# Kernel optimization log

Measured on AMD Instinct MI355X. Metric: run time of the kernel, lower is better.

## Reference

```python
import jax, jax.numpy as jnp
import numpy as np

D_MODEL = 1024
N_HEADS = 16
HEAD_DIM = D_MODEL // N_HEADS  # 64


def _rotate_half(x):
    x1, x2 = jnp.split(x, 2, axis=-1)
    return jnp.concatenate((-x2, x1), axis=-1)


def setup_inputs() -> dict:
    key = jax.random.key(0)
    ks = jax.random.split(key, 9)
    B, S = 2, 2048
    sc = 1.0 / np.sqrt(D_MODEL)
    return {
        "x": jax.random.normal(ks[0], (B, S, D_MODEL), dtype=jnp.float32),
        "Wq": jax.random.normal(ks[1], (D_MODEL, D_MODEL), dtype=jnp.float32) * sc,
        "bq": jax.random.normal(ks[2], (D_MODEL,), dtype=jnp.float32) * 0.02,
        "Wk": jax.random.normal(ks[3], (D_MODEL, D_MODEL), dtype=jnp.float32) * sc,
        "bk": jax.random.normal(ks[4], (D_MODEL,), dtype=jnp.float32) * 0.02,
        "Wv": jax.random.normal(ks[5], (D_MODEL, D_MODEL), dtype=jnp.float32) * sc,
        "bv": jax.random.normal(ks[6], (D_MODEL,), dtype=jnp.float32) * 0.02,
        "Wo": jax.random.normal(ks[7], (D_MODEL, D_MODEL), dtype=jnp.float32) * sc,
        "bo": jax.random.normal(ks[8], (D_MODEL,), dtype=jnp.float32) * 0.02,
    }


def reference(x, Wq, bq, Wk, bk, Wv, bv, Wo, bo):
    B, S, _ = x.shape
    H, D = N_HEADS, HEAD_DIM
    # QKV projections -> [B, H, S, D]
    q = (x @ Wq + bq).reshape(B, S, H, D).transpose(0, 2, 1, 3)
    k = (x @ Wk + bk).reshape(B, S, H, D).transpose(0, 2, 1, 3)
    v = (x @ Wv + bv).reshape(B, S, H, D).transpose(0, 2, 1, 3)
    # Rotary embedding on head_dim
    inv_freq = 1.0 / (10000.0 ** (jnp.arange(0, D, 2, dtype=jnp.float32) / D))
    t = jnp.arange(S, dtype=jnp.float32)
    freqs = jnp.outer(t, inv_freq)                      # [S, D/2]
    emb = jnp.concatenate((freqs, freqs), axis=-1)      # [S, D]
    # Faithful to torch: cos/sin end up rank-5 [1,1,1,S,D], promoting q/k to [1,B,H,S,D]
    cos = jnp.cos(emb)[None, None, None]
    sin = jnp.sin(emb)[None, None, None]
    qe = q * cos + _rotate_half(q) * sin                # [1,B,H,S,D]
    ke = k * cos + _rotate_half(k) * sin                # [1,B,H,S,D]
    scores = jnp.matmul(qe, jnp.swapaxes(ke, -1, -2)) / np.sqrt(D).astype(np.float32)  # [1,B,H,S,S]
    attn = jax.nn.softmax(scores, axis=-1)
    out = jnp.matmul(attn, v)                           # [1,B,H,S,D] (v broadcast)
    # Faithful replication of torch transpose(1,2).contiguous().view(B,S,d_model)
    out = out.transpose(0, 2, 1, 3, 4).reshape(B, S, H * D)
    return out @ Wo + bo
```

## Files before the change

kernel.cpp:

```cpp
#include <hip/hip_runtime.h>
#include <hip/hip_bf16.h>
#include <stdint.h>

typedef __bf16 bf16;
typedef __bf16 bf16x8 __attribute__((ext_vector_type(8)));
typedef __bf16 bf16x4 __attribute__((ext_vector_type(4)));
typedef float  f32x4  __attribute__((ext_vector_type(4)));
typedef int    i32x4  __attribute__((ext_vector_type(4)));

#define MFMA16(a, b, c) __builtin_amdgcn_mfma_f32_16x16x32_bf16((a), (b), (c), 0, 0, 0)

#define GLOAD16(gp, lp) __builtin_amdgcn_global_load_lds(                     \
    (__attribute__((address_space(1))) void*)(gp),                            \
    (__attribute__((address_space(3))) void*)(lp), 16, 0, 0)


__global__ __launch_bounds__(256) void k_prep(
    const float* __restrict__ x,
    const float* __restrict__ Wq, const float* __restrict__ Wk,
    const float* __restrict__ Wv, const float* __restrict__ Wo,
    bf16* __restrict__ xb, bf16* __restrict__ wqkvt, bf16* __restrict__ wot,
    float* __restrict__ ct, float* __restrict__ st) {
    __shared__ float t[32][33];
    const int bid = blockIdx.x, tid = threadIdx.x;
    if (bid < 4096) {
        const int i = bid * 256 + tid;
        float4 v = ((const float4*)x)[i];
        bf16x4 o;
        o[0] = (bf16)v.x; o[1] = (bf16)v.y; o[2] = (bf16)v.z; o[3] = (bf16)v.w;
        ((bf16x4*)xb)[i] = o;
    } else if (bid < 4352) {
        const int i = (bid - 4096) * 256 + tid;
        const int s = i >> 5, j = i & 31;
        const float inv = expf(-(float)j * (9.210340371976184f / 32.0f));
        const float a = (float)s * inv;
        ct[i] = cosf(a);
        st[i] = sinf(a);
    } else {
        const int wb = bid - 4352;
        const int z = wb >> 10, tb = wb & 1023;
        const float* src = (z == 0) ? Wq : (z == 1) ? Wk : (z == 2) ? Wv : Wo;
        bf16* dst = (z < 3) ? wqkvt + (size_t)z * 1024 * 1024 : wot;
        const int bx = (tb & 31) * 32, by = (tb >> 5) * 32;
        const int tx = tid & 31, ty = tid >> 5;
#pragma unroll
        for (int i = 0; i < 32; i += 8)
            t[ty + i][tx] = src[(size_t)(by + ty + i) * 1024 + bx + tx];
        __syncthreads();
#pragma unroll
        for (int i = 0; i < 32; i += 8)
            dst[(size_t)(bx + ty + i) * 1024 + by + tx] = (bf16)t[tx][ty + i];
    }
}

__global__ __launch_bounds__(512) void k_gemm_qkv(
    const bf16* __restrict__ X, const bf16* __restrict__ Wt,
    const float* __restrict__ bq, const float* __restrict__ bk,
    const float* __restrict__ bv,
    const float* __restrict__ ct, const float* __restrict__ st,
    bf16* __restrict__ qbuf, bf16* __restrict__ kbuf, bf16* __restrict__ vtb) {
    __shared__ __align__(16) bf16 As[2 * 16384];
    __shared__ __align__(16) bf16 Bs[2 * 16384];
    f32x4 acc[8][4] = {};

    const int wg = blockIdx.x;
    const int sw = (wg & 7) * 24 + (wg >> 3);
    const int m0 = (sw / 12) * 256, n0 = (sw % 12) * 256;

    const int tid = threadIdx.x;
    const int w = tid >> 6, lane = tid & 63;
    const int wm = w >> 2, wn = w & 3;
    const int l15 = lane & 15, l4 = lane >> 4;
    const int skol = 8 * ((lane & 7) ^ (lane >> 3));
    const int c0   = (8 * l4) ^ (8 * (l15 & 7));

    const bf16* Ap = X  + (size_t)(m0 + (tid >> 3)) * 1024 + skol;
    const bf16* Bp = Wt + (size_t)(n0 + (tid >> 3)) * 1024 + skol;
    bf16* Ad = As + tid * 8;
    bf16* Bd = Bs + tid * 8;
    const bf16* pA0 = As + (wm * 128 + l15) * 64 + c0;
    const bf16* pA1 = As + (wm * 128 + l15) * 64 + (c0 ^ 32);
    const bf16* pB0 = Bs + (wn * 64 + l15) * 64 + c0;
    const bf16* pB1 = Bs + (wn * 64 + l15) * 64 + (c0 ^ 32);

#define ASTG(B, kt) do {                                                     \
        GLOAD16(Ap + (kt),          Ad + (B) * 16384);                       \
        GLOAD16(Ap + 65536 + (kt),  Ad + (B) * 16384 + 4096);                \
        GLOAD16(Ap + 131072 + (kt), Ad + (B) * 16384 + 8192);                \
        GLOAD16(Ap + 196608 + (kt), Ad + (B) * 16384 + 12288);               \
    } while (0)
#define BSTG(B, kt) do {                                                     \
        GLOAD16(Bp + (kt),          Bd + (B) * 16384);                       \
        GLOAD16(Bp + 65536 + (kt),  Bd + (B) * 16384 + 4096);                \
        GLOAD16(Bp + 131072 + (kt), Bd + (B) * 16384 + 8192);                \
        GLOAD16(Bp + 196608 + (kt), Bd + (B) * 16384 + 12288);               \
    } while (0)

#define QTILE(t, B) do {                                                      \
        asm volatile("s_waitcnt vmcnt(0)" ::: "memory");                      \
        __builtin_amdgcn_s_barrier();                                         \
        bf16x8 af[8][2], bfv[4][2];                                           \
             \
        _Pragma("unroll")                                                     \
        for (int m = 0; m < 4; ++m) {                                         \
            af[m][0] = *(const bf16x8*)(pA0 + (B) * 16384 + m * 1024);        \
            af[m][1] = *(const bf16x8*)(pA1 + (B) * 16384 + m * 1024);        \
        }                                                                     \
        _Pragma("unroll")                                                     \
        for (int n = 0; n < 2; ++n) {                                         \
            bfv[n][0] = *(const bf16x8*)(pB0 + (B) * 16384 + n * 1024);       \
            bfv[n][1] = *(const bf16x8*)(pB1 + (B) * 16384 + n * 1024);       \
        }                                                                     \
        if ((t) < 15) ASTG((B) ^ 1, ((t) + 1) * 64);                          \
        __builtin_amdgcn_s_setprio(1);                                        \
        _Pragma("unroll")                                                     \
        for (int m = 0; m < 4; ++m)                                           \
            _Pragma("unroll")                                                 \
            for (int n = 0; n < 2; ++n) {                                     \
                acc[m][n] = MFMA16(af[m][0], bfv[n][0], acc[m][n]);           \
                acc[m][n] = MFMA16(af[m][1], bfv[n][1], acc[m][n]);           \
            }                                                                 \
        __builtin_amdgcn_s_setprio(0);                                        \
        __builtin_amdgcn_s_barrier();                                         \
                       \
        _Pragma("unroll")                                                     \
        for (int n = 2; n < 4; ++n) {                                         \
            bfv[n][0] = *(const bf16x8*)(pB0 + (B) * 16384 + n * 1024);       \
            bfv[n][1] = *(const bf16x8*)(pB1 + (B) * 16384 + n * 1024);       \
        }                                                                     \
        if ((t) < 15) BSTG((B) ^ 1, ((t) + 1) * 64);                          \
        __builtin_amdgcn_s_setprio(1);                                        \
        _Pragma("unroll")                                                     \
        for (int m = 0; m < 4; ++m)                                           \
            _Pragma("unroll")                                                 \
            for (int n = 2; n < 4; ++n) {                                     \
                acc[m][n] = MFMA16(af[m][0], bfv[n][0], acc[m][n]);           \
                acc[m][n] = MFMA16(af[m][1], bfv[n][1], acc[m][n]);           \
            }                                                                 \
        __builtin_amdgcn_s_setprio(0);                                        \
        __builtin_amdgcn_s_barrier();                                         \
                                      \
        _Pragma("unroll")                                                     \
        for (int m = 4; m < 8; ++m) {                                         \
            af[m][0] = *(const bf16x8*)(pA0 + (B) * 16384 + m * 1024);        \
            af[m][1] = *(const bf16x8*)(pA1 + (B) * 16384 + m * 1024);        \
        }                                                                     \
        __builtin_amdgcn_s_setprio(1);                                        \
        _Pragma("unroll")                                                     \
        for (int m = 4; m < 8; ++m)                                           \
            _Pragma("unroll")                                                 \
            for (int n = 2; n < 4; ++n) {                                     \
                acc[m][n] = MFMA16(af[m][0], bfv[n][0], acc[m][n]);           \
                acc[m][n] = MFMA16(af[m][1], bfv[n][1], acc[m][n]);           \
            }                                                                 \
        __builtin_amdgcn_s_setprio(0);                                        \
        __builtin_amdgcn_s_barrier();                                         \
                     \
        __builtin_amdgcn_s_setprio(1);                                        \
        _Pragma("unroll")                                                     \
        for (int m = 4; m < 8; ++m)                                           \
            _Pragma("unroll")                                                 \
            for (int n = 0; n < 2; ++n) {                                     \
                acc[m][n] = MFMA16(af[m][0], bfv[n][0], acc[m][n]);           \
                acc[m][n] = MFMA16(af[m][1], bfv[n][1], acc[m][n]);           \
            }                                                                 \
        __builtin_amdgcn_s_setprio(0);                                        \
    } while (0)

    ASTG(0, 0);
    BSTG(0, 0);
    for (int t = 0; t < 16; t += 2) {
        QTILE(t, 0);
        QTILE(t + 1, 1);
    }
#undef QTILE
#undef BSTG
#undef ASTG

    const int featbase = n0 + wn * 64;
    const int kind = featbase >> 10;
    const int col0 = featbase & 1023;
    const int h = col0 >> 6;
    const float* bias = (kind == 0) ? bq : (kind == 1) ? bk : bv;
    const float oscale = (kind == 0) ? 0.18033688011112042f : 1.0f;

#pragma unroll
    for (int m = 0; m < 8; ++m) {
#pragma unroll
        for (int j = 0; j < 4; ++j) {
            const int tok = m0 + wm * 128 + 16 * m + 4 * l4 + j;
            const int b = tok >> 11, s = tok & 2047;
            float vals[4];
#pragma unroll
            for (int n = 0; n < 4; ++n)
                vals[n] = acc[m][n][j] + bias[col0 + 16 * n + l15];
            if (kind < 2) {
                bf16* dst = (kind == 0) ? qbuf : kbuf;
                const size_t base = ((size_t)((b * 16 + h) * 2048 + s)) * 64;
#pragma unroll
                for (int n = 0; n < 4; ++n) {
                    const int dd = 16 * n + l15;
                    const int jr = dd & 31;
                    const float c = ct[s * 32 + jr], sn = st[s * 32 + jr];
                    const float other = vals[n ^ 2];
                    const float rot = (dd < 32) ? -other : other;
                    dst[base + dd] = (bf16)((vals[n] * c + rot * sn) * oscale);
                }
            } else {
                const int sp = (s & ~63) | ((s & 0x1C) << 1) | ((s & 0x20) >> 3) | (s & 3);
#pragma unroll
                for (int n = 0; n < 4; ++n) {
                    const int dd = 16 * n + l15;
                    vtb[((size_t)((b * 16 + h) * 64 + dd)) * 2048 + sp] = (bf16)vals[n];
                }
            }
        }
    }
}

__global__ __launch_bounds__(512) void k_attn(const bf16* __restrict__ qbuf,
                                              const bf16* __restrict__ kbuf,
                                              const bf16* __restrict__ vtb,
                                              bf16* __restrict__ ob) {
    __shared__ __align__(16) bf16 smem[2 * 2 * 2 * 4096];

    const int tid = threadIdx.x, w = tid >> 6, lane = tid & 63;
    const int team = w >> 2, wt = w & 3;
    const int l15 = lane & 15, l4 = lane >> 4;

    const int sid = blockIdx.x;
    const int bh  = (sid & 7) * 4 + ((sid >> 3) >> 4);
    const int qb0 = ((sid >> 3) & 15) * 128;
    const int b = bh >> 4, h = bh & 15;

    const bf16* qp = qbuf + ((size_t)bh * 2048 + qb0 + wt * 32 + l15) * 64 + 8 * l4;
    i32x4 qr00 = *(const i32x4*)qp;
    i32x4 qr01 = *(const i32x4*)(qp + 32);
    i32x4 qr10 = *(const i32x4*)(qp + 16 * 64);
    i32x4 qr11 = *(const i32x4*)(qp + 16 * 64 + 32);
    asm volatile("" :: "v"(qr00), "v"(qr01), "v"(qr10), "v"(qr11));
    asm volatile("s_waitcnt vmcnt(0)" ::: "memory");
    bf16x8 aq[2][2];
    aq[0][0] = __builtin_bit_cast(bf16x8, qr00);
    aq[0][1] = __builtin_bit_cast(bf16x8, qr01);
    aq[1][0] = __builtin_bit_cast(bf16x8, qr10);
    aq[1][1] = __builtin_bit_cast(bf16x8, qr11);

    bf16x8 ones;
#pragma unroll
    for (int i = 0; i < 8; ++i) ones[i] = (bf16)1.0f;

    f32x4 ao[2][4] = {};
    f32x4 lacc[2] = {};
    const f32x4 zf = {0.f, 0.f, 0.f, 0.f};

    const int r8   = lane >> 3;
    const int skol = 8 * ((lane & 7) ^ r8);
    const int rdb  = l15 * 64 + 32 * ((l15 >> 2) & 1) + 8 * (l4 ^ (l15 & 3));
    const bf16* kp = kbuf + (size_t)bh * 131072 + (size_t)team * 65536
                   + (size_t)(wt * 8 + r8) * 64 + skol;
    const bf16* vp = vtb  + (size_t)bh * 131072 + (size_t)(wt * 8 + r8) * 2048
                   + team * 1024 + skol;
    bf16* sK = smem + team * 16384;
    bf16* sV = smem + team * 16384 + 8192;
    const bf16* pK0 = sK + rdb;
    const bf16* pK1 = sK + (rdb ^ 32);
    const bf16* pV0 = sV + rdb;
    const bf16* pV1 = sV + (rdb ^ 32);

#define STAGE(B, t) do {                                                  \
        GLOAD16(kp + (size_t)(t) * 4096,        sK + (B) * 4096 + wt * 512);        \
        GLOAD16(kp + (size_t)(t) * 4096 + 2048, sK + (B) * 4096 + 2048 + wt * 512); \
        GLOAD16(vp + (t) * 64,                  sV + (B) * 4096 + wt * 512);        \
        GLOAD16(vp + 65536 + (t) * 64,          sV + (B) * 4096 + 2048 + wt * 512); \
    } while (0)

#define TILE(t, B) do {                                                       \
        asm volatile("s_waitcnt vmcnt(0)" ::: "memory");                      \
        __builtin_amdgcn_s_barrier();                                         \
        if ((t) < 15) STAGE((B) ^ 1, (t) + 1);                                \
        bf16x8 kfr[2][4], vfr[2][4];                                          \
        _Pragma("unroll")                                                     \
        for (int n = 0; n < 4; ++n) {                                         \
            kfr[0][n] = *(const bf16x8*)(pK0 + (B) * 4096 + n * 1024);        \
            kfr[1][n] = *(const bf16x8*)(pK1 + (B) * 4096 + n * 1024);        \
            vfr[0][n] = *(const bf16x8*)(pV0 + (B) * 4096 + n * 1024);        \
            vfr[1][n] = *(const bf16x8*)(pV1 + (B) * 4096 + n * 1024);        \
        }                                                                     \
        f32x4 sc[2][4];                                                       \
        __builtin_amdgcn_s_setprio(1);                                        \
        _Pragma("unroll")                                                     \
        for (int n = 0; n < 4; ++n) {                                         \
            sc[0][n] = MFMA16(kfr[0][n], aq[0][0], zf);                       \
            sc[1][n] = MFMA16(kfr[0][n], aq[1][0], zf);                       \
        }                                                                     \
        _Pragma("unroll")                                                     \
        for (int n = 0; n < 4; ++n) {                                         \
            sc[0][n] = MFMA16(kfr[1][n], aq[0][1], sc[0][n]);                 \
            sc[1][n] = MFMA16(kfr[1][n], aq[1][1], sc[1][n]);                 \
        }                                                                     \
        __builtin_amdgcn_s_setprio(0);                                        \
                  \
        bf16x8 ap[2][2];                                                      \
        _Pragma("unroll")                                                     \
        for (int f = 0; f < 2; ++f) {                                         \
            float e0[4], e1[4], e2[4], e3[4];                                 \
            _Pragma("unroll")                                                 \
            for (int r = 0; r < 4; ++r) {                                     \
                asm("v_exp_f32 %0, %1" : "=v"(e0[r]) : "v"(sc[f][0][r]));     \
                asm("v_exp_f32 %0, %1" : "=v"(e1[r]) : "v"(sc[f][1][r]));     \
                asm("v_exp_f32 %0, %1" : "=v"(e2[r]) : "v"(sc[f][2][r]));     \
                asm("v_exp_f32 %0, %1" : "=v"(e3[r]) : "v"(sc[f][3][r]));     \
            }                                                                 \
            unsigned q0, q1, q2, q3, q4, q5, q6, q7;                          \
            asm("v_cvt_pk_bf16_f32 %0, %1, %2" : "=v"(q0) : "v"(e0[0]), "v"(e0[1])); \
            asm("v_cvt_pk_bf16_f32 %0, %1, %2" : "=v"(q1) : "v"(e0[2]), "v"(e0[3])); \
            asm("v_cvt_pk_bf16_f32 %0, %1, %2" : "=v"(q2) : "v"(e2[0]), "v"(e2[1])); \
            asm("v_cvt_pk_bf16_f32 %0, %1, %2" : "=v"(q3) : "v"(e2[2]), "v"(e2[3])); \
            asm("v_cvt_pk_bf16_f32 %0, %1, %2" : "=v"(q4) : "v"(e1[0]), "v"(e1[1])); \
            asm("v_cvt_pk_bf16_f32 %0, %1, %2" : "=v"(q5) : "v"(e1[2]), "v"(e1[3])); \
            asm("v_cvt_pk_bf16_f32 %0, %1, %2" : "=v"(q6) : "v"(e3[0]), "v"(e3[1])); \
            asm("v_cvt_pk_bf16_f32 %0, %1, %2" : "=v"(q7) : "v"(e3[2]), "v"(e3[3])); \
            i32x4 w0 = {(int)q0, (int)q1, (int)q2, (int)q3};                  \
            i32x4 w1 = {(int)q4, (int)q5, (int)q6, (int)q7};                  \
            ap[f][0] = __builtin_bit_cast(bf16x8, w0);                        \
            ap[f][1] = __builtin_bit_cast(bf16x8, w1);                        \
        }                                                                     \
        __builtin_amdgcn_s_setprio(1);                                        \
        lacc[0] = MFMA16(ap[0][0], ones, lacc[0]);                            \
        lacc[0] = MFMA16(ap[0][1], ones, lacc[0]);                            \
        lacc[1] = MFMA16(ap[1][0], ones, lacc[1]);                            \
        lacc[1] = MFMA16(ap[1][1], ones, lacc[1]);                            \
        _Pragma("unroll")                                                     \
        for (int kk = 0; kk < 2; ++kk)                                        \
            _Pragma("unroll")                                                 \
            for (int n = 0; n < 4; ++n) {                                     \
                ao[0][n] = MFMA16(ap[0][kk], vfr[kk][n], ao[0][n]);           \
                ao[1][n] = MFMA16(ap[1][kk], vfr[kk][n], ao[1][n]);           \
            }                                                                 \
        __builtin_amdgcn_s_setprio(0);                                        \
    } while (0)

    STAGE(0, 0);
    for (int t = 0; t < 16; t += 2) {
        TILE(t, 0);
        TILE(t + 1, 1);
    }
#undef TILE
#undef STAGE

    float* mO = (float*)(smem + 16384);
    float* mL = (float*)smem;
    __syncthreads();
    if (team == 1) {
#pragma unroll
        for (int f = 0; f < 2; ++f) {
#pragma unroll
            for (int j = 0; j < 4; ++j) {
                const int row = wt * 32 + f * 16 + 4 * l4 + j;
#pragma unroll
                for (int n = 0; n < 4; ++n)
                    mO[row * 64 + 16 * n + l15] = ao[f][n][j];
                if (l15 == 0) mL[row] = lacc[f][j];
            }
        }
    }
    __syncthreads();
    if (team == 0) {
#pragma unroll
        for (int f = 0; f < 2; ++f) {
#pragma unroll
            for (int j = 0; j < 4; ++j) {
                const int row = wt * 32 + f * 16 + 4 * l4 + j;
                const float inv = 1.0f / (lacc[f][j] + mL[row]);
                const int s = qb0 + row;
                const size_t base = ((size_t)(h * 256 + b * 128 + (s >> 4))) * 1024
                                  + (s & 15) * 64;
#pragma unroll
                for (int n = 0; n < 4; ++n)
                    ob[base + 16 * n + l15] =
                        (bf16)((ao[f][n][j] + mO[row * 64 + 16 * n + l15]) * inv);
            }
        }
    }
}

__global__ __launch_bounds__(256) void k_gemm_out(const bf16* __restrict__ O,
                                                  const bf16* __restrict__ Wt,
                                                  const float* __restrict__ bo,
                                                  float* __restrict__ out) {
    __shared__ __align__(16) bf16 As[3 * 4096];
    __shared__ __align__(16) bf16 Bs[3 * 2048];
    f32x4 acc[4][2] = {};

    const int nwg = gridDim.x * gridDim.y;
    const int wg  = blockIdx.y * gridDim.x + blockIdx.x;
    const int sw  = (wg & 7) * (nwg >> 3) + (wg >> 3);
    const int m0 = (sw / gridDim.x) * 128, n0 = (sw % gridDim.x) * 64;

    const int tid  = threadIdx.x;
    const int w    = tid >> 6, lane = tid & 63;
    const int wr   = (w >> 1) * 64, wc = (w & 1) * 32;
    const int l15  = lane & 15, l4 = lane >> 4;
    const int srow = w * 16 + (lane >> 2);
    const int skol = 8 * ((lane & 3) ^ ((lane >> 3) & 3));
    const int rdb  = l15 * 32 + 8 * (l4 ^ ((l15 >> 1) & 3));
    const bf16* Ap = O  + (size_t)(m0 + srow) * 1024 + skol;
    const bf16* Bp = Wt + (size_t)(n0 + srow) * 1024 + skol;

#define OSTAGE(B, kt) do {                                                   \
        GLOAD16(Ap + (kt),         As + (B) * 4096 + w * 512);               \
        GLOAD16(Ap + 65536 + (kt), As + (B) * 4096 + 2048 + w * 512);        \
        GLOAD16(Bp + (kt),         Bs + (B) * 2048 + w * 512);               \
    } while (0)

#define OCOMP(B) do {                                                        \
        bf16x8 af[4], bfv[2];                                                \
        _Pragma("unroll")                                                    \
        for (int m = 0; m < 4; ++m)                                          \
            af[m] = *(const bf16x8*)(As + (B) * 4096 + (wr + 16 * m) * 32 + rdb); \
        _Pragma("unroll")                                                    \
        for (int n = 0; n < 2; ++n)                                          \
            bfv[n] = *(const bf16x8*)(Bs + (B) * 2048 + (wc + 16 * n) * 32 + rdb); \
        __builtin_amdgcn_s_setprio(1);                                       \
        _Pragma("unroll")                                                    \
        for (int m = 0; m < 4; ++m)                                          \
            _Pragma("unroll")                                                \
            for (int n = 0; n < 2; ++n)                                      \
                acc[m][n] = MFMA16(af[m], bfv[n], acc[m][n]);                \
        __builtin_amdgcn_s_setprio(0);                                       \
    } while (0)

    OSTAGE(0, 0);
    OSTAGE(1, 32);
    for (int i = 0; i < 30; i += 3) {
        asm volatile("s_waitcnt vmcnt(3)" ::: "memory");
        __builtin_amdgcn_s_barrier();
        OSTAGE(2, (i + 2) * 32);
        OCOMP(0);
        asm volatile("s_waitcnt vmcnt(3)" ::: "memory");
        __builtin_amdgcn_s_barrier();
        OSTAGE(0, (i + 3) * 32);
        OCOMP(1);
        asm volatile("s_waitcnt vmcnt(3)" ::: "memory");
        __builtin_amdgcn_s_barrier();
        OSTAGE(1, (i + 4) * 32);
        OCOMP(2);
    }
    asm volatile("s_waitcnt vmcnt(3)" ::: "memory");
    __builtin_amdgcn_s_barrier();
    OCOMP(0);
    asm volatile("s_waitcnt vmcnt(0)" ::: "memory");
    __builtin_amdgcn_s_barrier();
    OCOMP(1);
#undef OCOMP
#undef OSTAGE

#pragma unroll
    for (int m = 0; m < 4; ++m) {
#pragma unroll
        for (int j = 0; j < 4; ++j) {
            const int tok = m0 + wr + 16 * m + 4 * l4 + j;
#pragma unroll
            for (int n = 0; n < 2; ++n) {
                const int feat = n0 + wc + 16 * n + l15;
                out[(size_t)tok * 1024 + feat] = acc[m][n][j] + bo[feat];
            }
        }
    }
}

extern "C" void kernel_launch(void* const* d_in, const int* in_sizes, int n_in,
                              void* d_out, int out_size, void* d_ws, size_t ws_size,
                              hipStream_t stream) {
    (void)in_sizes; (void)n_in; (void)out_size; (void)ws_size;
    const float* x  = (const float*)d_in[0];
    const float* Wq = (const float*)d_in[1];
    const float* bq = (const float*)d_in[2];
    const float* Wk = (const float*)d_in[3];
    const float* bk = (const float*)d_in[4];
    const float* Wv = (const float*)d_in[5];
    const float* bv = (const float*)d_in[6];
    const float* Wo = (const float*)d_in[7];
    const float* bo = (const float*)d_in[8];
    float* out = (float*)d_out;

    char* p = (char*)d_ws;
    bf16* xb    = (bf16*)p;  p += (size_t)4096 * 1024 * 2;
    bf16* wqkvt = (bf16*)p;  p += (size_t)3072 * 1024 * 2;
    bf16* wot   = (bf16*)p;  p += (size_t)1024 * 1024 * 2;
    bf16* qbuf  = (bf16*)p;  p += (size_t)32 * 2048 * 64 * 2;
    bf16* kbuf  = (bf16*)p;  p += (size_t)32 * 2048 * 64 * 2;
    bf16* vtb   = (bf16*)p;  p += (size_t)32 * 64 * 2048 * 2;
    float* ct   = (float*)p; p += (size_t)2048 * 32 * 4;
    float* st   = (float*)p; p += (size_t)2048 * 32 * 4;
    bf16* obuf  = xb;

    k_prep<<<dim3(8448), dim3(256), 0, stream>>>(x, Wq, Wk, Wv, Wo,
                                                 xb, wqkvt, wot, ct, st);
    k_gemm_qkv<<<dim3(192), dim3(512), 0, stream>>>(xb, wqkvt, bq, bk, bv,
                                                    ct, st, qbuf, kbuf, vtb);
    k_attn<<<dim3(512), dim3(512), 0, stream>>>(qbuf, kbuf, vtb, obuf);
    k_gemm_out<<<dim3(16, 32), dim3(256), 0, stream>>>(obuf, wot, bo, out);
}
```

Measured before the change: 129.4 us.

## Restructure QKV GEMM mainloop into finer-grained half-tile staged pipeline

```diff
diff --git a/kernel.cpp b/kernel.cpp
--- a/kernel.cpp
+++ b/kernel.cpp
@@ -71,7 +71,7 @@
     const int w = tid >> 6, lane = tid & 63;
     const int wm = w >> 2, wn = w & 3;
     const int l15 = lane & 15, l4 = lane >> 4;
-    const int skol = 8 * ((lane & 7) ^ (lane >> 3));
+    const int skol = 8 * ((tid & 7) ^ ((tid >> 3) & 7));
     const int c0   = (8 * l4) ^ (8 * (l15 & 7));
 
     const bf16* Ap = X  + (size_t)(m0 + (tid >> 3)) * 1024 + skol;
@@ -83,99 +83,97 @@
     const bf16* pB0 = Bs + (wn * 64 + l15) * 64 + c0;
     const bf16* pB1 = Bs + (wn * 64 + l15) * 64 + (c0 ^ 32);
 
-#define ASTG(B, kt) do {                                                     \
-        GLOAD16(Ap + (kt),          Ad + (B) * 16384);                       \
-        GLOAD16(Ap + 65536 + (kt),  Ad + (B) * 16384 + 4096);                \
-        GLOAD16(Ap + 131072 + (kt), Ad + (B) * 16384 + 8192);                \
-        GLOAD16(Ap + 196608 + (kt), Ad + (B) * 16384 + 12288);               \
-    } while (0)
-#define BSTG(B, kt) do {                                                     \
-        GLOAD16(Bp + (kt),          Bd + (B) * 16384);                       \
-        GLOAD16(Bp + 65536 + (kt),  Bd + (B) * 16384 + 4096);                \
-        GLOAD16(Bp + 131072 + (kt), Bd + (B) * 16384 + 8192);                \
-        GLOAD16(Bp + 196608 + (kt), Bd + (B) * 16384 + 12288);               \
-    } while (0)
-
-#define QTILE(t, B) do {                                                      \
-        asm volatile("s_waitcnt vmcnt(0)" ::: "memory");                      \
-        __builtin_amdgcn_s_barrier();                                         \
-        bf16x8 af[8][2], bfv[4][2];                                           \
-             \
-        _Pragma("unroll")                                                     \
-        for (int m = 0; m < 4; ++m) {                                         \
-            af[m][0] = *(const bf16x8*)(pA0 + (B) * 16384 + m * 1024);        \
-            af[m][1] = *(const bf16x8*)(pA1 + (B) * 16384 + m * 1024);        \
-        }                                                                     \
-        _Pragma("unroll")                                                     \
-        for (int n = 0; n < 2; ++n) {                                         \
-            bfv[n][0] = *(const bf16x8*)(pB0 + (B) * 16384 + n * 1024);       \
-            bfv[n][1] = *(const bf16x8*)(pB1 + (B) * 16384 + n * 1024);       \
-        }                                                                     \
-        if ((t) < 15) ASTG((B) ^ 1, ((t) + 1) * 64);                          \
+#define STG_A(S, H, KT) do {                                                  \
+        GLOAD16(Ap + (size_t)((H) * 128) * 1024 + (KT) * 64,                  \
+                Ad + (S) * 16384 + (H) * 8192);                               \
+        GLOAD16(Ap + (size_t)((H) * 128 + 64) * 1024 + (KT) * 64,             \
+                Ad + (S) * 16384 + (H) * 8192 + 4096);                        \
+    } while (0)
+#define STG_B(S, H, KT) do {                                                  \
+        GLOAD16(Bp + (size_t)((H) * 128) * 1024 + (KT) * 64,                  \
+                Bd + (S) * 16384 + (H) * 8192);                               \
+        GLOAD16(Bp + (size_t)((H) * 128 + 64) * 1024 + (KT) * 64,             \
+                Bd + (S) * 16384 + (H) * 8192 + 4096);                        \
+    } while (0)
+
+#define RD_A03(S) _Pragma("unroll")                                           \
+    for (int m = 0; m < 4; ++m) {                                             \
+        af[m][0] = *(const bf16x8*)(pA0 + (S) * 16384 + m * 1024);            \
+        af[m][1] = *(const bf16x8*)(pA1 + (S) * 16384 + m * 1024);            \
+    }
+#define RD_A47(S) _Pragma("unroll")                                           \
+    for (int m = 4; m < 8; ++m) {                                             \
+        af[m][0] = *(const bf16x8*)(pA0 + (S) * 16384 + m * 1024);            \
+        af[m][1] = *(const bf16x8*)(pA1 + (S) * 16384 + m * 1024);            \
+    }
+#define RD_B01(S) _Pragma("unroll")                                           \
+    for (int n = 0; n < 2; ++n) {                                             \
+        bfv[n][0] = *(const bf16x8*)(pB0 + (S) * 16384 + n * 1024);           \
+        bfv[n][1] = *(const bf16x8*)(pB1 + (S) * 16384 + n * 1024);           \
+    }
+#define RD_B23(S) _Pragma("unroll")                                           \
+    for (int n = 2; n < 4; ++n) {                                             \
+        bfv[n][0] = *(const bf16x8*)(pB0 + (S) * 16384 + n * 1024);           \
+        bfv[n][1] = *(const bf16x8*)(pB1 + (S) * 16384 + n * 1024);           \
+    }
+#define MMQ(MLO, NLO) do {                                                    \
         __builtin_amdgcn_s_setprio(1);                                        \
         _Pragma("unroll")                                                     \
-        for (int m = 0; m < 4; ++m)                                           \
+        for (int m = (MLO); m < (MLO) + 4; ++m)                               \
             _Pragma("unroll")                                                 \
-            for (int n = 0; n < 2; ++n) {                                     \
+            for (int n = (NLO); n < (NLO) + 2; ++n) {                         \
                 acc[m][n] = MFMA16(af[m][0], bfv[n][0], acc[m][n]);           \
                 acc[m][n] = MFMA16(af[m][1], bfv[n][1], acc[m][n]);           \
             }                                                                 \
         __builtin_amdgcn_s_setprio(0);                                        \
-        __builtin_amdgcn_s_barrier();                                         \
-                       \
-        _Pragma("unroll")                                                     \
-        for (int n = 2; n < 4; ++n) {                                         \
-            bfv[n][0] = *(const bf16x8*)(pB0 + (B) * 16384 + n * 1024);       \
-            bfv[n][1] = *(const bf16x8*)(pB1 + (B) * 16384 + n * 1024);       \
-        }                                                                     \
-        if ((t) < 15) BSTG((B) ^ 1, ((t) + 1) * 64);                          \
-        __builtin_amdgcn_s_setprio(1);                                        \
-        _Pragma("unroll")                                                     \
-        for (int m = 0; m < 4; ++m)                                           \
-            _Pragma("unroll")                                                 \
-            for (int n = 2; n < 4; ++n) {                                     \
-                acc[m][n] = MFMA16(af[m][0], bfv[n][0], acc[m][n]);           \
-                acc[m][n] = MFMA16(af[m][1], bfv[n][1], acc[m][n]);           \
-            }                                                                 \
-        __builtin_amdgcn_s_setprio(0);                                        \
-        __builtin_amdgcn_s_barrier();                                         \
-                                      \
-        _Pragma("unroll")                                                     \
-        for (int m = 4; m < 8; ++m) {                                         \
-            af[m][0] = *(const bf16x8*)(pA0 + (B) * 16384 + m * 1024);        \
-            af[m][1] = *(const bf16x8*)(pA1 + (B) * 16384 + m * 1024);        \
-        }                                                                     \
-        __builtin_amdgcn_s_setprio(1);                                        \
-        _Pragma("unroll")                                                     \
-        for (int m = 4; m < 8; ++m)                                           \
-            _Pragma("unroll")                                                 \
-            for (int n = 2; n < 4; ++n) {                                     \
-                acc[m][n] = MFMA16(af[m][0], bfv[n][0], acc[m][n]);           \
-                acc[m][n] = MFMA16(af[m][1], bfv[n][1], acc[m][n]);           \
-            }                                                                 \
-        __builtin_amdgcn_s_setprio(0);                                        \
-        __builtin_amdgcn_s_barrier();                                         \
-                     \
-        __builtin_amdgcn_s_setprio(1);                                        \
-        _Pragma("unroll")                                                     \
-        for (int m = 4; m < 8; ++m)                                           \
-            _Pragma("unroll")                                                 \
-            for (int n = 0; n < 2; ++n) {                                     \
-                acc[m][n] = MFMA16(af[m][0], bfv[n][0], acc[m][n]);           \
-                acc[m][n] = MFMA16(af[m][1], bfv[n][1], acc[m][n]);           \
-            }                                                                 \
-        __builtin_amdgcn_s_setprio(0);                                        \
-    } while (0)
-
-    ASTG(0, 0);
-    BSTG(0, 0);
-    for (int t = 0; t < 16; t += 2) {
-        QTILE(t, 0);
-        QTILE(t + 1, 1);
-    }
-#undef QTILE
-#undef BSTG
-#undef ASTG
+    } while (0)
+#define BAR() __builtin_amdgcn_s_barrier()
+
+    STG_B(0, 0, 0); STG_B(0, 1, 0); STG_A(0, 0, 0); STG_A(0, 1, 0);
+    STG_B(1, 0, 1); STG_A(1, 0, 1);
+    asm volatile("s_waitcnt vmcnt(4)" ::: "memory");
+    BAR();
+
+    for (int t = 0; t < 8; ++t) {
+        const bool more = (t < 7);
+        bf16x8 af[8][2], bfv[4][2];
+        RD_A03(0); RD_B01(0);
+        STG_B(1, 1, 2 * t + 1);
+        BAR(); MMQ(0, 0); BAR();
+        RD_B23(0);
+        STG_A(1, 1, 2 * t + 1);
+        BAR(); MMQ(0, 2); BAR();
+        RD_A47(0);
+        if (more) STG_B(0, 0, 2 * t + 2);
+        BAR(); MMQ(4, 2); BAR();
+        if (more) {
+            STG_B(0, 1, 2 * t + 2);
+            asm volatile("s_waitcnt vmcnt(4)" ::: "memory");
+        } else {
+            asm volatile("s_waitcnt vmcnt(0)" ::: "memory");
+        }
+        BAR(); MMQ(4, 0); BAR();
+        RD_A03(1); RD_B01(1);
+        if (more) STG_A(0, 0, 2 * t + 2);
+        BAR(); MMQ(0, 0); BAR();
+        RD_B23(1);
+        if (more) STG_A(0, 1, 2 * t + 2);
+        BAR(); MMQ(0, 2); BAR();
+        RD_A47(1);
+        if (more) STG_B(1, 0, 2 * t + 3);
+        BAR(); MMQ(4, 2); BAR();
+        if (more) STG_A(1, 0, 2 * t + 3);
+        asm volatile("s_waitcnt vmcnt(4)" ::: "memory");
+        BAR(); MMQ(4, 0); BAR();
+    }
+#undef BAR
+#undef MMQ
+#undef RD_B23
+#undef RD_B01
+#undef RD_A47
+#undef RD_A03
+#undef STG_B
+#undef STG_A
 
     const int featbase = n0 + wn * 64;
     const int kind = featbase >> 10;
```

After: 132.3 us. 2.3% more time.
